# Performance work log

Measured on AMD Instinct MI355X. Metric: run time of the kernel, lower is better.

The kernel has to match this reference:

```python
import jax, jax.numpy as jnp
import numpy as np

D_K = 128
SCALE = 1.0 / np.sqrt(D_K).astype(np.float32)


def setup_inputs() -> dict:
    key = jax.random.key(0)
    kq, kk, kv = jax.random.split(key, 3)
    B, S, D = 8, 2048, D_K
    Q = jax.random.normal(kq, (B, S, D), dtype=jnp.float32)
    K = jax.random.normal(kk, (B, S, D), dtype=jnp.float32)
    V = jax.random.normal(kv, (B, S, D), dtype=jnp.float32)
    # causal mask: 1 = attend, 0 = block (per docstring semantics)
    mask = jnp.tril(jnp.ones((S, S), dtype=jnp.int32))
    return {"Q": Q, "K": K, "V": V, "mask": mask}


def reference(Q, K, V, mask):
    # scores: (B, S, S)
    scores = jnp.einsum("bqd,bkd->bqk", Q, K) * SCALE
    scores = jnp.where(mask == 0, -jnp.inf, scores)
    attention_weights = jax.nn.softmax(scores, axis=-1)
    output = jnp.einsum("bqk,bkd->bqd", attention_weights, V)
    return (output, attention_weights)
```

## Files before the change

### kernel.cpp

```cpp
#include <hip/hip_runtime.h>
#include <stdint.h>

#define BATCH 8
#define SEQ 2048
#define DH 128
#define QT 32
#define KT 64

static constexpr float SCALE_F = 0.08838834764831843f;

using bf16x8 = __attribute__((ext_vector_type(8))) short;
using f32x4  = __attribute__((ext_vector_type(4))) float;

__device__ inline unsigned short f2bf(float f) {
  unsigned u = __float_as_uint(f);
  u += 0x7fff + ((u >> 16) & 1);
  return (unsigned short)(u >> 16);
}

__device__ inline void gload_lds16(const void* g, void* l) {
  __builtin_amdgcn_global_load_lds(
      (const __attribute__((address_space(1))) void*)g,
      (__attribute__((address_space(3))) void*)l, 16, 0, 0);
}

extern "C" __global__ void __launch_bounds__(256)
convert_qk(const float4* __restrict__ Q, const float4* __restrict__ K,
           ushort4* __restrict__ Qb, ushort4* __restrict__ Kb) {
  int i = blockIdx.x * 256 + threadIdx.x;
  float4 q = Q[i];
  float4 k = K[i];
  ushort4 uq, uk;
  uq.x = f2bf(q.x); uq.y = f2bf(q.y); uq.z = f2bf(q.z); uq.w = f2bf(q.w);
  uk.x = f2bf(k.x); uk.y = f2bf(k.y); uk.z = f2bf(k.z); uk.w = f2bf(k.w);
  Qb[i] = uq;
  int r = i >> 5;
  int byte = (i & 31) * 8;
  int sbyte = byte ^ ((r & 7) << 4);
  Kb[(size_t)r * 32 + (sbyte >> 3)] = uk;
}

extern "C" __global__ void __launch_bounds__(256)
convert_v(const float* __restrict__ V, unsigned short* __restrict__ Vt) {
  __shared__ __align__(16) unsigned short L[DH][72];
  const int b = blockIdx.x >> 5;
  const int st = blockIdx.x & 31;
  const int s0 = st * 64;
  const int tid = threadIdx.x;
  const float* Vb = V + ((size_t)b * SEQ + s0) * DH;
#pragma unroll
  for (int it = 0; it < 8; ++it) {
    int f = (it * 256 + tid) * 4;
    int r = f >> 7, d0 = f & 127;
    float4 v = *(const float4*)(Vb + f);
    L[d0 + 0][r] = f2bf(v.x);
    L[d0 + 1][r] = f2bf(v.y);
    L[d0 + 2][r] = f2bf(v.z);
    L[d0 + 3][r] = f2bf(v.w);
  }
  __syncthreads();
  const int d = tid >> 1, h = tid & 1;
  unsigned short* dstb = Vt + ((size_t)b * DH + d) * SEQ + s0;
  const uint4* src = (const uint4*)&L[d][h * 32];
#pragma unroll
  for (int j = 0; j < 4; ++j) {
    int u = h * 4 + j;
    ((uint4*)dstb)[u ^ (d & 7)] = src[j];
  }
}

__global__ __launch_bounds__(256, 2) void attn_one(
    const unsigned short* __restrict__ Qbf, const unsigned short* __restrict__ Kbf,
    const unsigned short* __restrict__ Vtg,
    float* __restrict__ Og, float* __restrict__ Wg) {
  __shared__ __align__(16) unsigned short Ks[2][KT][128];
  __shared__ __align__(16) unsigned short Vs[2][DH][64];
  __shared__ __align__(16) unsigned short Ps[QT][72];
  __shared__ __align__(16) float Psf[QT][68];
  __shared__ float red[4][QT];

  const int tid = threadIdx.x;
  const int lane = tid & 63;
  const int w = tid >> 6;
  const int l15 = lane & 15;
  const int quad = lane >> 4;
  const int swz = (l15 & 7) << 4;

  const int b = blockIdx.x & 7;
  const int t = 63 - (blockIdx.x >> 3);
  const int q0 = t * QT;
  const int ntk = t / 2 + 1;

  const unsigned short* Qbb = Qbf + (size_t)b * SEQ * DH;
  const unsigned short* Kbb = Kbf + (size_t)b * SEQ * DH;
  const unsigned short* Vtb = Vtg + (size_t)b * DH * SEQ;
  float* Ob = Og + (size_t)b * SEQ * DH;
  float* Wb = Wg + (size_t)b * SEQ * SEQ;

  auto stageK = [&](int buf, int k0) {
#pragma unroll
    for (int it = 0; it < 4; ++it) {
      const unsigned short* g = Kbb + (size_t)k0 * DH + (it * 256 + tid) * 8;
      unsigned short* l = &Ks[buf][0][0] + (it * 256 + w * 64) * 8;
      gload_lds16(g, l);
    }
  };
  auto stageV = [&](int buf, int k0) {
#pragma unroll
    for (int it = 0; it < 4; ++it) {
      int f = it * 256 + tid;
      int d = f >> 3, u = f & 7;
      const unsigned short* g = Vtb + (size_t)d * SEQ + k0 + u * 8;
      unsigned short* l = &Vs[buf][0][0] + (it * 256 + w * 64) * 8;
      gload_lds16(g, l);
    }
  };

  {
    const int c0f = ntk * KT;
    const int len = SEQ - c0f;
    if (len > 0) {
      const float4 z4 = {0.f, 0.f, 0.f, 0.f};
      for (int r = 0; r < QT; ++r) {
        float* row = Wb + (size_t)(q0 + r) * SEQ + c0f;
        for (int c = tid * 4; c < len; c += 1024) *(float4*)(row + c) = z4;
      }
    }
  }

  bf16x8 qf0[4], qf1[4];
#pragma unroll
  for (int ks = 0; ks < 4; ++ks) {
    qf0[ks] = *(const bf16x8*)(Qbb + (size_t)(q0 + l15) * DH + ks * 32 + quad * 8);
    qf1[ks] = *(const bf16x8*)(Qbb + (size_t)(q0 + 16 + l15) * DH + ks * 32 + quad * 8);
  }

  stageK(0, 0);
  __syncthreads();

  float rs0[4] = {0.f, 0.f, 0.f, 0.f};
  float rs1[4] = {0.f, 0.f, 0.f, 0.f};
  int cur = 0;
  for (int kt = 0; kt < ntk; ++kt) {
    if (kt + 1 < ntk) stageK(cur ^ 1, (kt + 1) * KT);
    f32x4 a0 = {0.f, 0.f, 0.f, 0.f};
    f32x4 a1 = {0.f, 0.f, 0.f, 0.f};
#pragma unroll
    for (int ks = 0; ks < 4; ++ks) {
      const int cb = ((ks * 64 + quad * 16) ^ swz) >> 1;
      bf16x8 kb = *(const bf16x8*)(&Ks[cur][0][0] + (w * 16 + l15) * 128 + cb);
      a0 = __builtin_amdgcn_mfma_f32_16x16x32_bf16(qf0[ks], kb, a0, 0, 0, 0);
      a1 = __builtin_amdgcn_mfma_f32_16x16x32_bf16(qf1[ks], kb, a1, 0, 0, 0);
    }
    const int kcol = kt * KT + w * 16 + l15;
#pragma unroll
    for (int r = 0; r < 4; ++r) {
      const int row0 = q0 + quad * 4 + r;
      const int row1 = row0 + 16;
      rs0[r] += (kcol <= row0) ? __expf(a0[r] * SCALE_F) : 0.f;
      rs1[r] += (kcol <= row1) ? __expf(a1[r] * SCALE_F) : 0.f;
    }
    __syncthreads();
    cur ^= 1;
  }

  stageK(0, 0);
  stageV(0, 0);

#pragma unroll
  for (int m = 1; m <= 8; m <<= 1) {
#pragma unroll
    for (int r = 0; r < 4; ++r) {
      rs0[r] += __shfl_xor(rs0[r], m);
      rs1[r] += __shfl_xor(rs1[r], m);
    }
  }
  __syncthreads();
  if (l15 == 0) {
#pragma unroll
    for (int r = 0; r < 4; ++r) {
      red[w][quad * 4 + r] = rs0[r];
      red[w][16 + quad * 4 + r] = rs1[r];
    }
  }
  __syncthreads();
  float inv0[4], inv1[4];
#pragma unroll
  for (int r = 0; r < 4; ++r) {
    float s0 = red[0][quad * 4 + r] + red[1][quad * 4 + r] +
               red[2][quad * 4 + r] + red[3][quad * 4 + r];
    float s1 = red[0][16 + quad * 4 + r] + red[1][16 + quad * 4 + r] +
               red[2][16 + quad * 4 + r] + red[3][16 + quad * 4 + r];
    inv0[r] = 1.f / s0;
    inv1[r] = 1.f / s1;
  }

  f32x4 o00 = {0.f, 0.f, 0.f, 0.f}, o01 = {0.f, 0.f, 0.f, 0.f};
  f32x4 o10 = {0.f, 0.f, 0.f, 0.f}, o11 = {0.f, 0.f, 0.f, 0.f};
  const int srow = tid >> 3;
  const int sc0 = (tid & 7) * 8;
  cur = 0;
  for (int kt = 0; kt < ntk; ++kt) {
    if (kt + 1 < ntk) {
      stageK(cur ^ 1, (kt + 1) * KT);
      stageV(cur ^ 1, (kt + 1) * KT);
    }
    f32x4 a0 = {0.f, 0.f, 0.f, 0.f};
    f32x4 a1 = {0.f, 0.f, 0.f, 0.f};
#pragma unroll
    for (int ks = 0; ks < 4; ++ks) {
      const int cb = ((ks * 64 + quad * 16) ^ swz) >> 1;
      bf16x8 kb = *(const bf16x8*)(&Ks[cur][0][0] + (w * 16 + l15) * 128 + cb);
      a0 = __builtin_amdgcn_mfma_f32_16x16x32_bf16(qf0[ks], kb, a0, 0, 0, 0);
      a1 = __builtin_amdgcn_mfma_f32_16x16x32_bf16(qf1[ks], kb, a1, 0, 0, 0);
    }
    const int kcol = kt * KT + w * 16 + l15;
#pragma unroll
    for (int r = 0; r < 4; ++r) {
      const int row0 = q0 + quad * 4 + r;
      const int row1 = row0 + 16;
      float p0 = (kcol <= row0) ? __expf(a0[r] * SCALE_F) * inv0[r] : 0.f;
      float p1 = (kcol <= row1) ? __expf(a1[r] * SCALE_F) * inv1[r] : 0.f;
      Ps[quad * 4 + r][kcol - kt * KT] = f2bf(p0);
      Ps[16 + quad * 4 + r][kcol - kt * KT] = f2bf(p1);
      Psf[quad * 4 + r][kcol - kt * KT] = p0;
      Psf[16 + quad * 4 + r][kcol - kt * KT] = p1;
    }
    __syncthreads();
#pragma unroll
    for (int ks = 0; ks < 2; ++ks) {
      bf16x8 pa0 = *(const bf16x8*)&Ps[l15][ks * 32 + quad * 8];
      bf16x8 pa1 = *(const bf16x8*)&Ps[16 + l15][ks * 32 + quad * 8];
      const int cb = ((ks * 64 + quad * 16) ^ swz) >> 1;
      bf16x8 v0 = *(const bf16x8*)(&Vs[cur][0][0] + (w * 32 + l15) * 64 + cb);
      bf16x8 v1 = *(const bf16x8*)(&Vs[cur][0][0] + (w * 32 + 16 + l15) * 64 + cb);
      o00 = __builtin_amdgcn_mfma_f32_16x16x32_bf16(pa0, v0, o00, 0, 0, 0);
      o01 = __builtin_amdgcn_mfma_f32_16x16x32_bf16(pa0, v1, o01, 0, 0, 0);
      o10 = __builtin_amdgcn_mfma_f32_16x16x32_bf16(pa1, v0, o10, 0, 0, 0);
      o11 = __builtin_amdgcn_mfma_f32_16x16x32_bf16(pa1, v1, o11, 0, 0, 0);
    }
    {
      float4 x0 = *(const float4*)&Psf[srow][sc0];
      float4 x1 = *(const float4*)&Psf[srow][sc0 + 4];
      float* dst = Wb + (size_t)(q0 + srow) * SEQ + kt * KT + sc0;
      *(float4*)dst = x0;
      *(float4*)(dst + 4) = x1;
    }
    __syncthreads();
    cur ^= 1;
  }

#pragma unroll
  for (int r = 0; r < 4; ++r) {
    const int row0 = q0 + quad * 4 + r;
    const int row1 = row0 + 16;
    Ob[(size_t)row0 * DH + w * 32 + l15] = o00[r];
    Ob[(size_t)row0 * DH + w * 32 + 16 + l15] = o01[r];
    Ob[(size_t)row1 * DH + w * 32 + l15] = o10[r];
    Ob[(size_t)row1 * DH + w * 32 + 16 + l15] = o11[r];
  }
}

#define FQT 32
__global__ __launch_bounds__(256, 2) void attn_fb(
    const float* __restrict__ Qg, const float* __restrict__ Kg,
    const float* __restrict__ Vg, float* __restrict__ Og, float* __restrict__ Wg) {
  __shared__ __align__(16) unsigned short Qs[FQT][136];
  __shared__ __align__(16) unsigned short Ks[KT][136];
  __shared__ __align__(16) unsigned short Vs[DH][72];
  __shared__ __align__(16) unsigned short Ps[FQT][72];
  __shared__ float red[4][FQT];

  const int tid = threadIdx.x;
  const int lane = tid & 63;
  const int w = tid >> 6;
  const int l15 = lane & 15;
  const int quad = lane >> 4;

  const int b = blockIdx.x >> 5;
  const int z = blockIdx.x & 31;

  const float* Qgb = Qg + (size_t)b * SEQ * DH;
  const float* Kgb = Kg + (size_t)b * SEQ * DH;
  const float* Vgb = Vg + (size_t)b * SEQ * DH;
  float* Ob = Og + (size_t)b * SEQ * DH;
  float* Wb = Wg + (size_t)b * SEQ * SEQ;

  auto stageK = [&](int k0) {
#pragma unroll
    for (int it = 0; it < 8; ++it) {
      int f = (it * 256 + tid) * 4;
      int r = f >> 7, d0 = f & 127;
      float4 v = *(const float4*)(Kgb + (size_t)(k0 + r) * DH + d0);
      ushort4 u;
      u.x = f2bf(v.x); u.y = f2bf(v.y); u.z = f2bf(v.z); u.w = f2bf(v.w);
      *(ushort4*)&Ks[r][d0] = u;
    }
  };
  auto stageV = [&](int k0) {
#pragma unroll
    for (int it = 0; it < 8; ++it) {
      int f = (it * 256 + tid) * 4;
      int r = f >> 7, d0 = f & 127;
      float4 v = *(const float4*)(Vgb + (size_t)(k0 + r) * DH + d0);
      Vs[d0 + 0][r] = f2bf(v.x);
      Vs[d0 + 1][r] = f2bf(v.y);
      Vs[d0 + 2][r] = f2bf(v.z);
      Vs[d0 + 3][r] = f2bf(v.w);
    }
  };

  const int tiles[2] = {z, 63 - z};
  for (int ti = 0; ti < 2; ++ti) {
    const int t = tiles[ti];
    const int q0 = t * FQT;
    const int ntk = t / 2 + 1;
    {
      const int c0f = ntk * KT;
      const int len = SEQ - c0f;
      if (len > 0) {
        const float4 z4 = {0.f, 0.f, 0.f, 0.f};
        for (int r = 0; r < FQT; ++r) {
          float* row = Wb + (size_t)(q0 + r) * SEQ + c0f;
          for (int c = tid * 4; c < len; c += 1024) *(float4*)(row + c) = z4;
        }
      }
    }
    __syncthreads();
#pragma unroll
    for (int it = 0; it < 4; ++it) {
      int f = (it * 256 + tid) * 4;
      int r = f >> 7, d0 = f & 127;
      float4 v = *(const float4*)(Qgb + (size_t)(q0 + r) * DH + d0);
      ushort4 u;
      u.x = f2bf(v.x); u.y = f2bf(v.y); u.z = f2bf(v.z); u.w = f2bf(v.w);
      *(ushort4*)&Qs[r][d0] = u;
    }
    float rs0[4] = {0.f, 0.f, 0.f, 0.f};
    float rs1[4] = {0.f, 0.f, 0.f, 0.f};
    for (int kt = 0; kt < ntk; ++kt) {
      __syncthreads();
      stageK(kt * KT);
      __syncthreads();
      f32x4 a0 = {0.f, 0.f, 0.f, 0.f};
      f32x4 a1 = {0.f, 0.f, 0.f, 0.f};
#pragma unroll
      for (int ks = 0; ks < 4; ++ks) {
        bf16x8 qa0 = *(const bf16x8*)&Qs[l15][ks * 32 + quad * 8];
        bf16x8 qa1 = *(const bf16x8*)&Qs[16 + l15][ks * 32 + quad * 8];
        bf16x8 kb = *(const bf16x8*)&Ks[w * 16 + l15][ks * 32 + quad * 8];
        a0 = __builtin_amdgcn_mfma_f32_16x16x32_bf16(qa0, kb, a0, 0, 0, 0);
        a1 = __builtin_amdgcn_mfma_f32_16x16x32_bf16(qa1, kb, a1, 0, 0, 0);
      }
      const int kcol = kt * KT + w * 16 + l15;
#pragma unroll
      for (int r = 0; r < 4; ++r) {
        const int row0 = q0 + quad * 4 + r;
        const int row1 = row0 + 16;
        rs0[r] += (kcol <= row0) ? __expf(a0[r] * SCALE_F) : 0.f;
        rs1[r] += (kcol <= row1) ? __expf(a1[r] * SCALE_F) : 0.f;
      }
    }
#pragma unroll
    for (int m = 1; m <= 8; m <<= 1) {
#pragma unroll
      for (int r = 0; r < 4; ++r) {
        rs0[r] += __shfl_xor(rs0[r], m);
        rs1[r] += __shfl_xor(rs1[r], m);
      }
    }
    __syncthreads();
    if (l15 == 0) {
#pragma unroll
      for (int r = 0; r < 4; ++r) {
        red[w][quad * 4 + r] = rs0[r];
        red[w][16 + quad * 4 + r] = rs1[r];
      }
    }
    __syncthreads();
    float inv0[4], inv1[4];
#pragma unroll
    for (int r = 0; r < 4; ++r) {
      float s0 = red[0][quad * 4 + r] + red[1][quad * 4 + r] +
                 red[2][quad * 4 + r] + red[3][quad * 4 + r];
      float s1 = red[0][16 + quad * 4 + r] + red[1][16 + quad * 4 + r] +
                 red[2][16 + quad * 4 + r] + red[3][16 + quad * 4 + r];
      inv0[r] = 1.f / s0;
      inv1[r] = 1.f / s1;
    }
    f32x4 o00 = {0.f, 0.f, 0.f, 0.f}, o01 = {0.f, 0.f, 0.f, 0.f};
    f32x4 o10 = {0.f, 0.f, 0.f, 0.f}, o11 = {0.f, 0.f, 0.f, 0.f};
    for (int kt = 0; kt < ntk; ++kt) {
      __syncthreads();
      stageK(kt * KT);
      stageV(kt * KT);
      __syncthreads();
      f32x4 a0 = {0.f, 0.f, 0.f, 0.f};
      f32x4 a1 = {0.f, 0.f, 0.f, 0.f};
#pragma unroll
      for (int ks = 0; ks < 4; ++ks) {
        bf16x8 qa0 = *(const bf16x8*)&Qs[l15][ks * 32 + quad * 8];
        bf16x8 qa1 = *(const bf16x8*)&Qs[16 + l15][ks * 32 + quad * 8];
        bf16x8 kb = *(const bf16x8*)&Ks[w * 16 + l15][ks * 32 + quad * 8];
        a0 = __builtin_amdgcn_mfma_f32_16x16x32_bf16(qa0, kb, a0, 0, 0, 0);
        a1 = __builtin_amdgcn_mfma_f32_16x16x32_bf16(qa1, kb, a1, 0, 0, 0);
      }
      const int kcol = kt * KT + w * 16 + l15;
#pragma unroll
      for (int r = 0; r < 4; ++r) {
        const int row0 = q0 + quad * 4 + r;
        const int row1 = row0 + 16;
        float p0 = (kcol <= row0) ? __expf(a0[r] * SCALE_F) * inv0[r] : 0.f;
        float p1 = (kcol <= row1) ? __expf(a1[r] * SCALE_F) * inv1[r] : 0.f;
        Wb[(size_t)row0 * SEQ + kcol] = p0;
        Wb[(size_t)row1 * SEQ + kcol] = p1;
        Ps[quad * 4 + r][w * 16 + l15] = f2bf(p0);
        Ps[16 + quad * 4 + r][w * 16 + l15] = f2bf(p1);
      }
      __syncthreads();
#pragma unroll
      for (int ks = 0; ks < 2; ++ks) {
        bf16x8 pa0 = *(const bf16x8*)&Ps[l15][ks * 32 + quad * 8];
        bf16x8 pa1 = *(const bf16x8*)&Ps[16 + l15][ks * 32 + quad * 8];
        bf16x8 v0 = *(const bf16x8*)&Vs[w * 32 + l15][ks * 32 + quad * 8];
        bf16x8 v1 = *(const bf16x8*)&Vs[w * 32 + 16 + l15][ks * 32 + quad * 8];
        o00 = __builtin_amdgcn_mfma_f32_16x16x32_bf16(pa0, v0, o00, 0, 0, 0);
        o01 = __builtin_amdgcn_mfma_f32_16x16x32_bf16(pa0, v1, o01, 0, 0, 0);
        o10 = __builtin_amdgcn_mfma_f32_16x16x32_bf16(pa1, v0, o10, 0, 0, 0);
        o11 = __builtin_amdgcn_mfma_f32_16x16x32_bf16(pa1, v1, o11, 0, 0, 0);
      }
    }
#pragma unroll
    for (int r = 0; r < 4; ++r) {
      const int row0 = q0 + quad * 4 + r;
      const int row1 = row0 + 16;
      Ob[(size_t)row0 * DH + w * 32 + l15] = o00[r];
      Ob[(size_t)row0 * DH + w * 32 + 16 + l15] = o01[r];
      Ob[(size_t)row1 * DH + w * 32 + l15] = o10[r];
      Ob[(size_t)row1 * DH + w * 32 + 16 + l15] = o11[r];
    }
  }
}

extern "C" void kernel_launch(void* const* d_in, const int* in_sizes, int n_in,
                              void* d_out, int out_size, void* d_ws, size_t ws_size,
                              hipStream_t stream) {
  const float* Q = (const float*)d_in[0];
  const float* K = (const float*)d_in[1];
  const float* V = (const float*)d_in[2];
  float* Out = (float*)d_out;
  float* W = Out + (size_t)BATCH * SEQ * DH;

  const size_t nel = (size_t)BATCH * SEQ * DH;
  const size_t need = nel * 2 * 3;
  if (ws_size >= need) {
    unsigned short* Qbf = (unsigned short*)d_ws;
    unsigned short* Kbf = Qbf + nel;
    unsigned short* Vt = Kbf + nel;
    hipLaunchKernelGGL(convert_qk, dim3((unsigned)(nel / 4 / 256)), dim3(256), 0, stream,
                       (const float4*)Q, (const float4*)K, (ushort4*)Qbf, (ushort4*)Kbf);
    hipLaunchKernelGGL(convert_v, dim3(BATCH * (SEQ / 64)), dim3(256), 0, stream, V, Vt);
    hipLaunchKernelGGL(attn_one, dim3(BATCH * 64), dim3(256), 0, stream,
                       Qbf, Kbf, Vt, Out, W);
  } else {
    hipLaunchKernelGGL(attn_fb, dim3(BATCH * 32), dim3(256), 0, stream,
                       Q, K, V, Out, W);
  }
}
```

Measured before the change: 216.9 us.

## Split softmax row-sum pass into separate finer-grained kernel before PV kernel

New measurement: 220.0 us. Within noise of the previous version (+1.4%).

```diff
diff --git a/kernel.cpp b/kernel.cpp
--- a/kernel.cpp
+++ b/kernel.cpp
@@ -69,7 +69,84 @@
   }
 }
 
-__global__ __launch_bounds__(256, 2) void attn_one(
+__global__ __launch_bounds__(256, 4) void attn_sums(
+    const unsigned short* __restrict__ Qbf, const unsigned short* __restrict__ Kbf,
+    float* __restrict__ Wg) {
+  __shared__ __align__(16) unsigned short Ks[2][KT][128];
+  __shared__ float red[4][16];
+
+  const int tid = threadIdx.x;
+  const int lane = tid & 63;
+  const int w = tid >> 6;
+  const int l15 = lane & 15;
+  const int quad = lane >> 4;
+  const int swz = (l15 & 7) << 4;
+
+  const int b = blockIdx.x & 7;
+  const int z = blockIdx.x >> 3;
+  const int t = (z < 64) ? (127 - z) : (z - 64);
+  const int q0 = t * 16;
+  const int ntk = (t >> 2) + 1;
+
+  const unsigned short* Qbb = Qbf + (size_t)b * SEQ * DH;
+  const unsigned short* Kbb = Kbf + (size_t)b * SEQ * DH;
+  float* Wb = Wg + (size_t)b * SEQ * SEQ;
+
+  auto stageK = [&](int buf, int k0) {
+#pragma unroll
+    for (int it = 0; it < 4; ++it) {
+      const unsigned short* g = Kbb + (size_t)k0 * DH + (it * 256 + tid) * 8;
+      unsigned short* l = &Ks[buf][0][0] + (it * 256 + w * 64) * 8;
+      gload_lds16(g, l);
+    }
+  };
+
+  bf16x8 qf[4];
+#pragma unroll
+  for (int ks = 0; ks < 4; ++ks)
+    qf[ks] = *(const bf16x8*)(Qbb + (size_t)(q0 + l15) * DH + ks * 32 + quad * 8);
+
+  stageK(0, 0);
+  __syncthreads();
+
+  float rs[4] = {0.f, 0.f, 0.f, 0.f};
+  int cur = 0;
+  for (int kt = 0; kt < ntk; ++kt) {
+    if (kt + 1 < ntk) stageK(cur ^ 1, (kt + 1) * KT);
+    f32x4 a0 = {0.f, 0.f, 0.f, 0.f};
+#pragma unroll
+    for (int ks = 0; ks < 4; ++ks) {
+      const int cb = ((ks * 64 + quad * 16) ^ swz) >> 1;
+      bf16x8 kb = *(const bf16x8*)(&Ks[cur][0][0] + (w * 16 + l15) * 128 + cb);
+      a0 = __builtin_amdgcn_mfma_f32_16x16x32_bf16(qf[ks], kb, a0, 0, 0, 0);
+    }
+    const int kcol = kt * KT + w * 16 + l15;
+#pragma unroll
+    for (int r = 0; r < 4; ++r) {
+      const int row0 = q0 + quad * 4 + r;
+      rs[r] += (kcol <= row0) ? __expf(a0[r] * SCALE_F) : 0.f;
+    }
+    __syncthreads();
+    cur ^= 1;
+  }
+
+#pragma unroll
+  for (int m = 1; m <= 8; m <<= 1) {
+#pragma unroll
+    for (int r = 0; r < 4; ++r) rs[r] += __shfl_xor(rs[r], m);
+  }
+  if (l15 == 0) {
+#pragma unroll
+    for (int r = 0; r < 4; ++r) red[w][quad * 4 + r] = rs[r];
+  }
+  __syncthreads();
+  if (tid < 16) {
+    float s = red[0][tid] + red[1][tid] + red[2][tid] + red[3][tid];
+    Wb[(size_t)(q0 + tid) * SEQ + (SEQ - 1)] = 1.f / s;
+  }
+}
+
+__global__ __launch_bounds__(256, 2) void attn_pv(
     const unsigned short* __restrict__ Qbf, const unsigned short* __restrict__ Kbf,
     const unsigned short* __restrict__ Vtg,
     float* __restrict__ Og, float* __restrict__ Wg) {
@@ -77,7 +154,7 @@
   __shared__ __align__(16) unsigned short Vs[2][DH][64];
   __shared__ __align__(16) unsigned short Ps[QT][72];
   __shared__ __align__(16) float Psf[QT][68];
-  __shared__ float red[4][QT];
+  __shared__ float redv[QT];
 
   const int tid = threadIdx.x;
   const int lane = tid & 63;
@@ -87,7 +164,8 @@
   const int swz = (l15 & 7) << 4;
 
   const int b = blockIdx.x & 7;
-  const int t = 63 - (blockIdx.x >> 3);
+  const int z = blockIdx.x >> 3;
+  const int t = (z < 32) ? (63 - z) : (z - 32);
   const int q0 = t * QT;
   const int ntk = t / 2 + 1;
 
@@ -115,6 +193,15 @@
       gload_lds16(g, l);
     }
   };
+
+  if (tid < QT) redv[tid] = Wb[(size_t)(q0 + tid) * SEQ + (SEQ - 1)];
+  __syncthreads();
+  float inv0[4], inv1[4];
+#pragma unroll
+  for (int r = 0; r < 4; ++r) {
+    inv0[r] = redv[quad * 4 + r];
+    inv1[r] = redv[16 + quad * 4 + r];
+  }
 
   {
     const int c0f = ntk * KT;
@@ -136,70 +223,14 @@
   }
 
   stageK(0, 0);
+  stageV(0, 0);
   __syncthreads();
-
-  float rs0[4] = {0.f, 0.f, 0.f, 0.f};
-  float rs1[4] = {0.f, 0.f, 0.f, 0.f};
-  int cur = 0;
-  for (int kt = 0; kt < ntk; ++kt) {
-    if (kt + 1 < ntk) stageK(cur ^ 1, (kt + 1) * KT);
-    f32x4 a0 = {0.f, 0.f, 0.f, 0.f};
-    f32x4 a1 = {0.f, 0.f, 0.f, 0.f};
-#pragma unroll
-    for (int ks = 0; ks < 4; ++ks) {
-      const int cb = ((ks * 64 + quad * 16) ^ swz) >> 1;
-      bf16x8 kb = *(const bf16x8*)(&Ks[cur][0][0] + (w * 16 + l15) * 128 + cb);
-      a0 = __builtin_amdgcn_mfma_f32_16x16x32_bf16(qf0[ks], kb, a0, 0, 0, 0);
-      a1 = __builtin_amdgcn_mfma_f32_16x16x32_bf16(qf1[ks], kb, a1, 0, 0, 0);
-    }
-    const int kcol = kt * KT + w * 16 + l15;
-#pragma unroll
-    for (int r = 0; r < 4; ++r) {
-      const int row0 = q0 + quad * 4 + r;
-      const int row1 = row0 + 16;
-      rs0[r] += (kcol <= row0) ? __expf(a0[r] * SCALE_F) : 0.f;
-      rs1[r] += (kcol <= row1) ? __expf(a1[r] * SCALE_F) : 0.f;
-    }
-    __syncthreads();
-    cur ^= 1;
-  }
-
-  stageK(0, 0);
-  stageV(0, 0);
-
-#pragma unroll
-  for (int m = 1; m <= 8; m <<= 1) {
-#pragma unroll
-    for (int r = 0; r < 4; ++r) {
-      rs0[r] += __shfl_xor(rs0[r], m);
-      rs1[r] += __shfl_xor(rs1[r], m);
-    }
-  }
-  __syncthreads();
-  if (l15 == 0) {
-#pragma unroll
-    for (int r = 0; r < 4; ++r) {
-      red[w][quad * 4 + r] = rs0[r];
-      red[w][16 + quad * 4 + r] = rs1[r];
-    }
-  }
-  __syncthreads();
-  float inv0[4], inv1[4];
-#pragma unroll
-  for (int r = 0; r < 4; ++r) {
-    float s0 = red[0][quad * 4 + r] + red[1][quad * 4 + r] +
-               red[2][quad * 4 + r] + red[3][quad * 4 + r];
-    float s1 = red[0][16 + quad * 4 + r] + red[1][16 + quad * 4 + r] +
-               red[2][16 + quad * 4 + r] + red[3][16 + quad * 4 + r];
-    inv0[r] = 1.f / s0;
-    inv1[r] = 1.f / s1;
-  }
 
   f32x4 o00 = {0.f, 0.f, 0.f, 0.f}, o01 = {0.f, 0.f, 0.f, 0.f};
   f32x4 o10 = {0.f, 0.f, 0.f, 0.f}, o11 = {0.f, 0.f, 0.f, 0.f};
   const int srow = tid >> 3;
   const int sc0 = (tid & 7) * 8;
-  cur = 0;
+  int cur = 0;
   for (int kt = 0; kt < ntk; ++kt) {
     if (kt + 1 < ntk) {
       stageK(cur ^ 1, (kt + 1) * KT);
@@ -460,7 +491,9 @@
     hipLaunchKernelGGL(convert_qk, dim3((unsigned)(nel / 4 / 256)), dim3(256), 0, stream,
                        (const float4*)Q, (const float4*)K, (ushort4*)Qbf, (ushort4*)Kbf);
     hipLaunchKernelGGL(convert_v, dim3(BATCH * (SEQ / 64)), dim3(256), 0, stream, V, Vt);
-    hipLaunchKernelGGL(attn_one, dim3(BATCH * 64), dim3(256), 0, stream,
+    hipLaunchKernelGGL(attn_sums, dim3(BATCH * 128), dim3(256), 0, stream,
+                       Qbf, Kbf, W);
+    hipLaunchKernelGGL(attn_pv, dim3(BATCH * 64), dim3(256), 0, stream,
                        Qbf, Kbf, Vt, Out, W);
   } else {
     hipLaunchKernelGGL(attn_fb, dim3(BATCH * 32), dim3(256), 0, stream,
```
